# Kernel tuning notes

Hardware: AMD Instinct MI355X
Metric: run time of the kernel (lower is better)

Reference implementation:

```python
import jax, jax.numpy as jnp
import numpy as np

B, N, K, H = 2, 2048, 48, 128
NIN = 2 * H          # num_in = 2*num_hidden (ProteinMPNN wiring)
FF = 4 * H           # PositionWiseFeedForward hidden
SCALE = 30.0
EPS = 1e-5           # torch LayerNorm default eps


def _ln(x, g, b):
    m = jnp.mean(x, axis=-1, keepdims=True)
    v = jnp.mean((x - m) ** 2, axis=-1, keepdims=True)
    return (x - m) / jnp.sqrt(v + EPS) * g + b


def _gelu(x):
    return jax.nn.gelu(x, approximate=False)  # torch.nn.GELU default (erf)


def _lin(x, W, b):
    return x @ W + b


def setup_inputs() -> dict:
    key = jax.random.key(0)
    ks = jax.random.split(key, 24)
    s = 0.05
    inp = {
        "h_V": jax.random.normal(ks[0], (B, N, H), jnp.float32),
        "h_E": jax.random.normal(ks[1], (B, N, K, H), jnp.float32),
        "E_idx": jax.random.randint(ks[2], (B, N, K), 0, N, jnp.int64),
        "mask_V": jnp.ones((B, N), jnp.float32),
        "mask_attend": jnp.ones((B, N, K), jnp.float32),
        # message MLP (node update): W1 in = H + NIN = 3H
        "W1": jax.random.normal(ks[3], (3 * H, H), jnp.float32) * s,
        "b1": jnp.zeros((H,), jnp.float32),
        "W2": jax.random.normal(ks[4], (H, H), jnp.float32) * s,
        "b2": jnp.zeros((H,), jnp.float32),
        "W3": jax.random.normal(ks[5], (H, H), jnp.float32) * s,
        "b3": jnp.zeros((H,), jnp.float32),
        # PositionWiseFeedForward
        "Wd_in": jax.random.normal(ks[6], (H, FF), jnp.float32) * s,
        "bd_in": jnp.zeros((FF,), jnp.float32),
        "Wd_out": jax.random.normal(ks[7], (FF, H), jnp.float32) * s,
        "bd_out": jnp.zeros((H,), jnp.float32),
        # edge-update MLP: W11 in = H + NIN = 3H
        "W11": jax.random.normal(ks[8], (3 * H, H), jnp.float32) * s,
        "b11": jnp.zeros((H,), jnp.float32),
        "W12": jax.random.normal(ks[9], (H, H), jnp.float32) * s,
        "b12": jnp.zeros((H,), jnp.float32),
        "W13": jax.random.normal(ks[10], (H, H), jnp.float32) * s,
        "b13": jnp.zeros((H,), jnp.float32),
        # LayerNorms
        "n1g": jnp.ones((H,), jnp.float32), "n1b": jnp.zeros((H,), jnp.float32),
        "n2g": jnp.ones((H,), jnp.float32), "n2b": jnp.zeros((H,), jnp.float32),
        "n3g": jnp.ones((H,), jnp.float32), "n3b": jnp.zeros((H,), jnp.float32),
    }
    return inp


def reference(h_V, h_E, E_idx, mask_V, mask_attend,
              W1, b1, W2, b2, W3, b3,
              Wd_in, bd_in, Wd_out, bd_out,
              W11, b11, W12, b12, W13, b13,
              n1g, n1b, n2g, n2b, n3g, n3b):
    gather = jax.vmap(lambda hv, idx: hv[idx])  # [B,N,H],[B,N,K] -> [B,N,K,H]

    # --- node update: cat_neighbors_nodes + expand + 3-layer GELU MLP ---
    h_nb = gather(h_V, E_idx)                                   # [B,N,K,H]
    hV_exp = jnp.broadcast_to(h_V[:, :, None, :], h_nb.shape)   # [B,N,K,H]
    h_EV = jnp.concatenate([hV_exp, h_E, h_nb], axis=-1)        # [B,N,K,3H]
    h_msg = _lin(_gelu(_lin(_gelu(_lin(h_EV, W1, b1)), W2, b2)), W3, b3)
    h_msg = mask_attend[..., None] * h_msg
    dh = jnp.sum(h_msg, axis=-2) / SCALE                        # masked-sum reduce
    h_V = _ln(h_V + dh, n1g, n1b)

    # --- position-wise FFN ---
    dh = _lin(_gelu(_lin(h_V, Wd_in, bd_in)), Wd_out, bd_out)
    h_V = _ln(h_V + dh, n2g, n2b)
    h_V = mask_V[..., None] * h_V

    # --- edge update (not last layer) ---
    h_nb2 = gather(h_V, E_idx)
    hV_exp2 = jnp.broadcast_to(h_V[:, :, None, :], h_nb2.shape)
    h_EV2 = jnp.concatenate([hV_exp2, h_E, h_nb2], axis=-1)     # [B,N,K,3H]
    h_msg2 = _lin(_gelu(_lin(_gelu(_lin(h_EV2, W11, b11)), W12, b12)), W13, b13)
    h_E = _ln(h_E + h_msg2, n3g, n3b)
    return (h_V, h_E)
```

## Files before the change

### kernel.cpp

```cpp
#include <hip/hip_runtime.h>
#include <hip/hip_bf16.h>
#include <stdint.h>

#define XP2 264
#define MP 136
#define EPIP 132
#define FFP 520

typedef __attribute__((ext_vector_type(8))) short bf16x8;
typedef __attribute__((ext_vector_type(4))) float f32x4;

__device__ __forceinline__ f32x4 mfma16(bf16x8 a, bf16x8 b, f32x4 c) {
  return __builtin_amdgcn_mfma_f32_16x16x32_bf16(a, b, c, 0, 0, 0);
}

__device__ __forceinline__ uint16_t f2b(float f) {
  union { __hip_bfloat16 h; uint16_t u; } v;
  v.h = __float2bfloat16(f);
  return v.u;
}
__device__ __forceinline__ uint32_t pk2f(float a, float b) {
  union { __hip_bfloat162 h; uint32_t u; } v;
  v.h = __float22bfloat162_rn(make_float2(a, b));
  return v.u;
}
__device__ __forceinline__ float gelu_f(float x) {
  float u = __builtin_fmaf(x * x, 0.044715f, 1.0f);
  float e = __builtin_amdgcn_exp2f(-2.302585093f * x * u);
  return x * __builtin_amdgcn_rcpf(1.0f + e);
}

__global__ __launch_bounds__(256) void k_prep(
    const float* __restrict__ hV,
    const float* __restrict__ W1, const float* __restrict__ W2, const float* __restrict__ W3,
    const float* __restrict__ WdIn, const float* __restrict__ WdOut,
    const float* __restrict__ W11, const float* __restrict__ W12, const float* __restrict__ W13,
    uint16_t* __restrict__ hVb,
    uint16_t* __restrict__ W1t, uint16_t* __restrict__ W2t, uint16_t* __restrict__ W3t,
    uint16_t* __restrict__ WdInT, uint16_t* __restrict__ WdOutT,
    uint16_t* __restrict__ W11t, uint16_t* __restrict__ W12t, uint16_t* __restrict__ W13t) {
  int i = blockIdx.x * 256 + threadIdx.x;
  if (i < 524288) { hVb[i] = f2b(hV[i]); return; }
  int j = i - 524288;
  if (j < 49152) { int n = j / 384, k = j - n * 384; W1t[j] = f2b(W1[k * 128 + n]); return; }
  j -= 49152;
  if (j < 16384) { int n = j >> 7, k = j & 127; W2t[j] = f2b(W2[k * 128 + n]); return; }
  j -= 16384;
  if (j < 16384) { int n = j >> 7, k = j & 127; W3t[j] = f2b(W3[k * 128 + n]); return; }
  j -= 16384;
  if (j < 65536) { int n = j >> 7, k = j & 127; WdInT[j] = f2b(WdIn[k * 512 + n]); return; }
  j -= 65536;
  if (j < 65536) { int n = j >> 9, k = j & 511; WdOutT[j] = f2b(WdOut[k * 128 + n]); return; }
  j -= 65536;
  if (j < 49152) { int n = j / 384, k = j - n * 384; W11t[j] = f2b(W11[k * 128 + n]); return; }
  j -= 49152;
  if (j < 16384) { int n = j >> 7, k = j & 127; W12t[j] = f2b(W12[k * 128 + n]); return; }
  j -= 16384;
  if (j < 16384) { int n = j >> 7, k = j & 127; W13t[j] = f2b(W13[k * 128 + n]); return; }
}

__global__ __launch_bounds__(256) void k_vec(
    const uint16_t* __restrict__ Xb, const uint16_t* __restrict__ Wt,
    float* __restrict__ C) {
  const int tid = threadIdx.x;
  const int lane = tid & 63, w = tid >> 6, l15 = lane & 15, lg = lane >> 4;
  const int row0 = blockIdx.x * 64 + w * 16;
  f32x4 acc[8] = {};
#pragma unroll
  for (int ks = 0; ks < 4; ++ks) {
    bf16x8 a = *(const bf16x8*)(Xb + (row0 + l15) * 128 + ks * 32 + lg * 8);
#pragma unroll
    for (int j = 0; j < 8; ++j) {
      bf16x8 bb = *(const bf16x8*)(Wt + (j * 16 + l15) * 384 + ks * 32 + lg * 8);
      acc[j] = mfma16(a, bb, acc[j]);
    }
  }
#pragma unroll
  for (int j = 0; j < 8; ++j)
#pragma unroll
    for (int r = 0; r < 4; ++r)
      C[(row0 + lg * 4 + r) * 128 + j * 16 + l15] = acc[j][r];
}

#define BUILD_XT(GSRC)                                                              \
  do {                                                                              \
    for (int idx = tid; idx < 48 * 32; idx += 256) {                                \
      int k_ = idx >> 5;                                                            \
      int c_ = idx & 31;                                                            \
      uint4 v_;                                                                     \
      if (c_ < 16) {                                                                \
        const float* s_ = hE + (size_t)(bn * 48 + k_) * 128 + (c_ << 3);            \
        float4 f0_ = *(const float4*)s_;                                            \
        float4 f1_ = *(const float4*)(s_ + 4);                                      \
        v_ = make_uint4(pk2f(f0_.x, f0_.y), pk2f(f0_.z, f0_.w),                     \
                        pk2f(f1_.x, f1_.y), pk2f(f1_.z, f1_.w));                    \
      } else {                                                                      \
        v_ = *(const uint4*)((GSRC) + (size_t)nbr[k_] * 128 + ((c_ - 16) << 3));    \
      }                                                                             \
      *(uint4*)(xt + k_ * XP2 + (c_ << 3)) = v_;                                    \
    }                                                                               \
  } while (0)

#define LAYER256(WT, ACC)                                                           \
  do {                                                                              \
    const uint16_t* wr0_ = (WT) + (w * 32 + l15) * 384 + 128 + lg * 8;              \
    const uint16_t* wr1_ = wr0_ + 16 * 384;                                         \
    _Pragma("unroll 2") for (int ks = 0; ks < 8; ++ks) {                            \
      bf16x8 bA_ = *(const bf16x8*)(wr0_ + ks * 32);                                \
      bf16x8 bB_ = *(const bf16x8*)(wr1_ + ks * 32);                                \
      _Pragma("unroll") for (int m = 0; m < 3; ++m) {                               \
        bf16x8 a_ = *(const bf16x8*)(xt + (m * 16 + l15) * XP2 + ks * 32 + lg * 8); \
        ACC[m][0] = mfma16(a_, bA_, ACC[m][0]);                                     \
        ACC[m][1] = mfma16(a_, bB_, ACC[m][1]);                                     \
      }                                                                             \
    }                                                                               \
  } while (0)

#define LAYER128(WT, ASRC, ACC)                                                     \
  do {                                                                              \
    const uint16_t* wr0_ = (WT) + (w * 32 + l15) * 128 + lg * 8;                    \
    const uint16_t* wr1_ = wr0_ + 16 * 128;                                         \
    _Pragma("unroll") for (int ks = 0; ks < 4; ++ks) {                              \
      bf16x8 bA_ = *(const bf16x8*)(wr0_ + ks * 32);                                \
      bf16x8 bB_ = *(const bf16x8*)(wr1_ + ks * 32);                                \
      _Pragma("unroll") for (int m = 0; m < 3; ++m) {                               \
        bf16x8 a_ = *(const bf16x8*)((ASRC) + (m * 16 + l15) * MP + ks * 32 + lg * 8); \
        ACC[m][0] = mfma16(a_, bA_, ACC[m][0]);                                     \
        ACC[m][1] = mfma16(a_, bB_, ACC[m][1]);                                     \
      }                                                                              \
    }                                                                               \
  } while (0)

#define GSTORE(ACC, BIAS, DST)                                                      \
  do {                                                                              \
    float bA_ = (BIAS)[w * 32 + l15];                                               \
    float bB_ = (BIAS)[w * 32 + 16 + l15];                                          \
    _Pragma("unroll") for (int m = 0; m < 3; ++m)                                   \
    _Pragma("unroll") for (int r = 0; r < 4; ++r) {                                 \
      int row_ = m * 16 + lg * 4 + r;                                               \
      (DST)[row_ * MP + w * 32 + l15] = f2b(gelu_f(ACC[m][0][r] + bA_));            \
      (DST)[row_ * MP + w * 32 + 16 + l15] = f2b(gelu_f(ACC[m][1][r] + bB_));       \
    }                                                                               \
  } while (0)

#define ACC_INIT(ACC, CV)                                                           \
  do {                                                                              \
    float c0_ = (CV)[bn * 128 + w * 32 + l15];                                      \
    float c1_ = (CV)[bn * 128 + w * 32 + 16 + l15];                                 \
    _Pragma("unroll") for (int m = 0; m < 3; ++m) {                                 \
      ACC[m][0] = (f32x4){c0_, c0_, c0_, c0_};                                      \
      ACC[m][1] = (f32x4){c1_, c1_, c1_, c1_};                                      \
    }                                                                               \
  } while (0)

__global__ __launch_bounds__(256, 6) void k_node(
    const float* __restrict__ hV, const float* __restrict__ hE,
    const int* __restrict__ eidx, const float* __restrict__ maskA,
    const float* __restrict__ bias1, const float* __restrict__ bias2,
    const float* __restrict__ bias3,
    const float* __restrict__ g1, const float* __restrict__ be1,
    const uint16_t* __restrict__ hVb, const float* __restrict__ C1,
    const uint16_t* __restrict__ W1t, const uint16_t* __restrict__ W2t,
    const uint16_t* __restrict__ W3t,
    float* __restrict__ hV1, uint16_t* __restrict__ hV1b) {
  __shared__ __align__(16) unsigned char lds[26880];
  uint16_t* xt = (uint16_t*)lds;
  uint16_t* midA = (uint16_t*)lds;
  uint16_t* midB = (uint16_t*)(lds + 13056);
  int* nbr = (int*)(lds + 26112);
  float* dh = (float*)(lds + 26368);

  const int tid = threadIdx.x;
  const int lane = tid & 63;
  const int w = tid >> 6;
  const int l15 = lane & 15;
  const int lg = lane >> 4;
  const int bn = blockIdx.x;
  const int b = bn >> 11;

  if (tid < 48) nbr[tid] = (b << 11) + eidx[bn * 48 + tid];
  __syncthreads();

  BUILD_XT(hVb);
  __syncthreads();

  f32x4 acc1[3][2];
  ACC_INIT(acc1, C1);
  LAYER256(W1t, acc1);
  __syncthreads();
  GSTORE(acc1, bias1, midA);
  __syncthreads();

  f32x4 acc2[3][2] = {};
  LAYER128(W2t, midA, acc2);
  GSTORE(acc2, bias2, midB);
  __syncthreads();

  f32x4 acc3[3][2] = {};
  LAYER128(W3t, midB, acc3);

  {
    float bA = bias3[w * 32 + l15];
    float bB = bias3[w * 32 + 16 + l15];
    float s0 = 0.f, s1 = 0.f;
#pragma unroll
    for (int m = 0; m < 3; ++m)
#pragma unroll
      for (int r = 0; r < 4; ++r) {
        int row = m * 16 + lg * 4 + r;
        float mk = maskA[bn * 48 + row];
        s0 += (acc3[m][0][r] + bA) * mk;
        s1 += (acc3[m][1][r] + bB) * mk;
      }
    s0 += __shfl_xor(s0, 16); s0 += __shfl_xor(s0, 32);
    s1 += __shfl_xor(s1, 16); s1 += __shfl_xor(s1, 32);
    if (lg == 0) { dh[w * 32 + l15] = s0; dh[w * 32 + 16 + l15] = s1; }
  }
  __syncthreads();

  if (w == 0) {
    const float inv = 1.0f / 30.0f;
    float x0 = hV[bn * 128 + lane] + dh[lane] * inv;
    float x1 = hV[bn * 128 + 64 + lane] + dh[64 + lane] * inv;
    float s = x0 + x1, q = x0 * x0 + x1 * x1;
#pragma unroll
    for (int off = 1; off < 64; off <<= 1) {
      s += __shfl_xor(s, off);
      q += __shfl_xor(q, off);
    }
    float mean = s * (1.0f / 128.0f);
    float var = q * (1.0f / 128.0f) - mean * mean;
    float rstd = rsqrtf(var + 1e-5f);
    float y0 = (x0 - mean) * rstd * g1[lane] + be1[lane];
    float y1 = (x1 - mean) * rstd * g1[64 + lane] + be1[64 + lane];
    hV1[bn * 128 + lane] = y0;
    hV1[bn * 128 + 64 + lane] = y1;
    hV1b[bn * 128 + lane] = f2b(y0);
    hV1b[bn * 128 + 64 + lane] = f2b(y1);
  }
}

__global__ __launch_bounds__(256, 2) void k_ffn(
    const float* __restrict__ hV1, const uint16_t* __restrict__ hV1b,
    const float* __restrict__ maskV,
    const float* __restrict__ bdin, const float* __restrict__ bdout,
    const float* __restrict__ g2, const float* __restrict__ be2,
    const uint16_t* __restrict__ WdInT, const uint16_t* __restrict__ WdOutT,
    float* __restrict__ outV, uint16_t* __restrict__ hV2b) {
  __shared__ __align__(16) unsigned char lds[20992];
  uint16_t* xa = (uint16_t*)lds;
  uint16_t* mf = (uint16_t*)(lds + 4352);
  float* epi = (float*)(lds + 4352);

  const int tid = threadIdx.x;
  const int lane = tid & 63;
  const int w = tid >> 6;
  const int l15 = lane & 15;
  const int lg = lane >> 4;
  const int node0 = blockIdx.x * 16;

  {
    int row = tid >> 4, c = tid & 15;
    *(uint4*)(xa + row * 136 + (c << 3)) =
        *(const uint4*)(hV1b + (node0 + row) * 128 + (c << 3));
  }
  __syncthreads();

  f32x4 acc[8] = {};
  {
    const uint16_t* ar = xa + l15 * 136 + lg * 8;
#pragma unroll
    for (int ks = 0; ks < 4; ++ks) {
      bf16x8 a = *(const bf16x8*)(ar + ks * 32);
#pragma unroll
      for (int j = 0; j < 8; ++j) {
        bf16x8 bb = *(const bf16x8*)(WdInT + ((w * 8 + j) * 16 + l15) * 128 + ks * 32 + lg * 8);
        acc[j] = mfma16(a, bb, acc[j]);
      }
    }
  }
#pragma unroll
  for (int j = 0; j < 8; ++j) {
    int col = (w * 8 + j) * 16 + l15;
    float bs = bdin[col];
#pragma unroll
    for (int r = 0; r < 4; ++r) {
      int row = lg * 4 + r;
      mf[row * FFP + col] = f2b(gelu_f(acc[j][r] + bs));
    }
  }
  __syncthreads();

  f32x4 acc2[2] = {};
  {
    const uint16_t* mr = mf + l15 * FFP + lg * 8;
#pragma unroll 4
    for (int ks = 0; ks < 16; ++ks) {
      bf16x8 a = *(const bf16x8*)(mr + ks * 32);
#pragma unroll
      for (int t = 0; t < 2; ++t) {
        bf16x8 bb = *(const bf16x8*)(WdOutT + ((w * 2 + t) * 16 + l15) * 512 + ks * 32 + lg * 8);
        acc2[t] = mfma16(a, bb, acc2[t]);
      }
    }
  }
  __syncthreads();
#pragma unroll
  for (int t = 0; t < 2; ++t) {
    int col = (w * 2 + t) * 16 + l15;
    float bs = bdout[col];
#pragma unroll
    for (int r = 0; r < 4; ++r) {
      int row = lg * 4 + r;
      epi[row * EPIP + col] = acc2[t][r] + bs;
    }
  }
  __syncthreads();

#pragma unroll
  for (int rr = 0; rr < 4; ++rr) {
    int row = w * 4 + rr;
    int node = node0 + row;
    float x0 = epi[row * EPIP + lane] + hV1[node * 128 + lane];
    float x1 = epi[row * EPIP + 64 + lane] + hV1[node * 128 + 64 + lane];
    float s = x0 + x1, q = x0 * x0 + x1 * x1;
#pragma unroll
    for (int off = 1; off < 64; off <<= 1) {
      s += __shfl_xor(s, off);
      q += __shfl_xor(q, off);
    }
    float mean = s * (1.0f / 128.0f);
    float var = q * (1.0f / 128.0f) - mean * mean;
    float rstd = rsqrtf(var + 1e-5f);
    float mv = maskV[node];
    float y0 = mv * ((x0 - mean) * rstd * g2[lane] + be2[lane]);
    float y1 = mv * ((x1 - mean) * rstd * g2[64 + lane] + be2[64 + lane]);
    outV[node * 128 + lane] = y0;
    outV[node * 128 + 64 + lane] = y1;
    hV2b[node * 128 + lane] = f2b(y0);
    hV2b[node * 128 + 64 + lane] = f2b(y1);
  }
}

__global__ __launch_bounds__(256, 6) void k_edge(
    const float* __restrict__ hE, const int* __restrict__ eidx,
    const float* __restrict__ bias1, const float* __restrict__ bias2,
    const float* __restrict__ bias3,
    const float* __restrict__ g3, const float* __restrict__ be3,
    const uint16_t* __restrict__ hV2b, const float* __restrict__ C2,
    const uint16_t* __restrict__ W1t, const uint16_t* __restrict__ W2t,
    const uint16_t* __restrict__ W3t,
    float* __restrict__ outE) {
  __shared__ __align__(16) unsigned char lds[26304];
  uint16_t* xt = (uint16_t*)lds;
  uint16_t* midA = (uint16_t*)lds;
  uint16_t* midB = (uint16_t*)(lds + 13056);
  int* nbr = (int*)(lds + 26112);
  float* part_s = (float*)lds;
  float* part_q = (float*)(lds + 768);
  float* mstd = (float*)(lds + 1536);

  const int tid = threadIdx.x;
  const int lane = tid & 63;
  const int w = tid >> 6;
  const int l15 = lane & 15;
  const int lg = lane >> 4;
  const int bn = blockIdx.x;
  const int b = bn >> 11;

  if (tid < 48) nbr[tid] = (b << 11) + eidx[bn * 48 + tid];
  __syncthreads();

  BUILD_XT(hV2b);
  __syncthreads();

  f32x4 acc1[3][2];
  ACC_INIT(acc1, C2);
  LAYER256(W1t, acc1);
  __syncthreads();
  GSTORE(acc1, bias1, midA);
  __syncthreads();

  f32x4 acc2[3][2] = {};
  LAYER128(W2t, midA, acc2);
  GSTORE(acc2, bias2, midB);
  __syncthreads();

  f32x4 acc3[3][2] = {};
  LAYER128(W3t, midB, acc3);

  const float bA = bias3[w * 32 + l15];
  const float bB = bias3[w * 32 + 16 + l15];

  float xs0[3][4], xs1[3][4];
#pragma unroll
  for (int m = 0; m < 3; ++m)
#pragma unroll
    for (int r = 0; r < 4; ++r) {
      int row = m * 16 + lg * 4 + r;
      size_t e = (size_t)bn * 48 + row;
      xs0[m][r] = acc3[m][0][r] + bA + hE[e * 128 + w * 32 + l15];
      xs1[m][r] = acc3[m][1][r] + bB + hE[e * 128 + w * 32 + 16 + l15];
      float s = xs0[m][r] + xs1[m][r];
      float q = xs0[m][r] * xs0[m][r] + xs1[m][r] * xs1[m][r];
      s += __shfl_xor(s, 1); q += __shfl_xor(q, 1);
      s += __shfl_xor(s, 2); q += __shfl_xor(q, 2);
      s += __shfl_xor(s, 4); q += __shfl_xor(q, 4);
      s += __shfl_xor(s, 8); q += __shfl_xor(q, 8);
      if (l15 == 0) { part_s[row * 4 + w] = s; part_q[row * 4 + w] = q; }
    }
  __syncthreads();

  if (tid < 48) {
    float s = part_s[tid * 4] + part_s[tid * 4 + 1] + part_s[tid * 4 + 2] + part_s[tid * 4 + 3];
    float q = part_q[tid * 4] + part_q[tid * 4 + 1] + part_q[tid * 4 + 2] + part_q[tid * 4 + 3];
    float mean = s * (1.0f / 128.0f);
    float var = q * (1.0f / 128.0f) - mean * mean;
    mstd[tid * 2] = mean;
    mstd[tid * 2 + 1] = rsqrtf(var + 1e-5f);
  }
  __syncthreads();

  const float gA = g3[w * 32 + l15], beA = be3[w * 32 + l15];
  const float gB = g3[w * 32 + 16 + l15], beB = be3[w * 32 + 16 + l15];
#pragma unroll
  for (int m = 0; m < 3; ++m)
#pragma unroll
    for (int r = 0; r < 4; ++r) {
      int row = m * 16 + lg * 4 + r;
      size_t e = (size_t)bn * 48 + row;
      float mean = mstd[row * 2];
      float rstd = mstd[row * 2 + 1];
      outE[e * 128 + w * 32 + l15] = (xs0[m][r] - mean) * rstd * gA + beA;
      outE[e * 128 + w * 32 + 16 + l15] = (xs1[m][r] - mean) * rstd * gB + beB;
    }
}

extern "C" void kernel_launch(void* const* d_in, const int* in_sizes, int n_in,
                              void* d_out, int out_size, void* d_ws, size_t ws_size,
                              hipStream_t stream) {
  const float* hV = (const float*)d_in[0];
  const float* hE = (const float*)d_in[1];
  const int* eidx = (const int*)d_in[2];
  const float* maskV = (const float*)d_in[3];
  const float* maskA = (const float*)d_in[4];
  const float* W1 = (const float*)d_in[5];   const float* b1 = (const float*)d_in[6];
  const float* W2 = (const float*)d_in[7];   const float* b2 = (const float*)d_in[8];
  const float* W3 = (const float*)d_in[9];   const float* b3 = (const float*)d_in[10];
  const float* WdIn = (const float*)d_in[11];  const float* bdin = (const float*)d_in[12];
  const float* WdOut = (const float*)d_in[13]; const float* bdout = (const float*)d_in[14];
  const float* W11 = (const float*)d_in[15]; const float* b11 = (const float*)d_in[16];
  const float* W12 = (const float*)d_in[17]; const float* b12 = (const float*)d_in[18];
  const float* W13 = (const float*)d_in[19]; const float* b13 = (const float*)d_in[20];
  const float* n1g = (const float*)d_in[21]; const float* n1b = (const float*)d_in[22];
  const float* n2g = (const float*)d_in[23]; const float* n2b = (const float*)d_in[24];
  const float* n3g = (const float*)d_in[25]; const float* n3b = (const float*)d_in[26];

  char* ws = (char*)d_ws;
  uint16_t* hVb    = (uint16_t*)(ws + 0);
  uint16_t* W1t    = (uint16_t*)(ws + 1048576);
  uint16_t* W2t    = (uint16_t*)(ws + 1146880);
  uint16_t* W3t    = (uint16_t*)(ws + 1179648);
  uint16_t* WdInT  = (uint16_t*)(ws + 1212416);
  uint16_t* WdOutT = (uint16_t*)(ws + 1343488);
  uint16_t* W11t   = (uint16_t*)(ws + 1474560);
  uint16_t* W12t   = (uint16_t*)(ws + 1572864);
  uint16_t* W13t   = (uint16_t*)(ws + 1605632);
  float*    hV1    = (float*)(ws + 1638400);
  uint16_t* hV1b   = (uint16_t*)(ws + 3735552);
  uint16_t* hV2b   = (uint16_t*)(ws + 4784128);
  float*    C1     = (float*)(ws + 5832704);
  float*    C2     = (float*)(ws + 7929856);

  float* outV = (float*)d_out;
  float* outE = (float*)d_out + 524288;

  k_prep<<<3200, 256, 0, stream>>>(hV, W1, W2, W3, WdIn, WdOut, W11, W12, W13,
                                   hVb, W1t, W2t, W3t, WdInT, WdOutT, W11t, W12t, W13t);
  k_vec<<<64, 256, 0, stream>>>(hVb, W1t, C1);
  k_node<<<4096, 256, 0, stream>>>(hV, hE, eidx, maskA, b1, b2, b3, n1g, n1b,
                                   hVb, C1, W1t, W2t, W3t, hV1, hV1b);
  k_ffn<<<256, 256, 0, stream>>>(hV1, hV1b, maskV, bdin, bdout, n2g, n2b,
                                 WdInT, WdOutT, outV, hV2b);
  k_vec<<<64, 256, 0, stream>>>(hV2b, W11t, C2);
  k_edge<<<4096, 256, 0, stream>>>(hE, eidx, b11, b12, b13, n3g, n3b,
                                   hV2b, C2, W11t, W12t, W13t, outE);
}
```

Before: 226.1 us.

## Restructure node kernel to per-wave edge tiles with direct global operand loads

The node kernel is rewritten so each 192-thread block handles two nodes (96 edges). Each wave owns 32 edges and computes all 128 output channels in transposed form, loading hE and gathered neighbor rows directly from global memory into MFMA operands. This drops the shared LDS staging of the concatenated input and most block-wide barriers; intermediate activations go to per-wave LDS buffers. Layer-1 bias is folded into the precomputed per-node vector term in k_vec, which also affects the edge kernel. The trade-off is more accumulator registers per wave (8x2 tiles) and lower occupancy via launch bounds (192,3), plus a fragile div48 trick and hard-coded batch offset. Only a compiler fence, not a barrier, separates per-wave LDS writes and reads.

```diff
diff --git a/kernel.cpp b/kernel.cpp
--- a/kernel.cpp
+++ b/kernel.cpp
@@ -2,16 +2,21 @@
 #include <hip/hip_bf16.h>
 #include <stdint.h>
 
+#define MIDP 136
 #define XP2 264
 #define MP 136
+#define FFP 520
 #define EPIP 132
-#define FFP 520
 
 typedef __attribute__((ext_vector_type(8))) short bf16x8;
 typedef __attribute__((ext_vector_type(4))) float f32x4;
 
 __device__ __forceinline__ f32x4 mfma16(bf16x8 a, bf16x8 b, f32x4 c) {
   return __builtin_amdgcn_mfma_f32_16x16x32_bf16(a, b, c, 0, 0, 0);
+}
+
+__device__ __forceinline__ void lds_fence() {
+  asm volatile("" ::: "memory");
 }
 
 __device__ __forceinline__ uint16_t f2b(float f) {
@@ -28,6 +33,9 @@
   float u = __builtin_fmaf(x * x, 0.044715f, 1.0f);
   float e = __builtin_amdgcn_exp2f(-2.302585093f * x * u);
   return x * __builtin_amdgcn_rcpf(1.0f + e);
+}
+__device__ __forceinline__ int div48(int e) {
+  return (int)((((unsigned)e >> 4) * 0xAAABu) >> 17);
 }
 
 __global__ __launch_bounds__(256) void k_prep(
@@ -61,7 +69,7 @@
 
 __global__ __launch_bounds__(256) void k_vec(
     const uint16_t* __restrict__ Xb, const uint16_t* __restrict__ Wt,
-    float* __restrict__ C) {
+    const float* __restrict__ bias, float* __restrict__ C) {
   const int tid = threadIdx.x;
   const int lane = tid & 63, w = tid >> 6, l15 = lane & 15, lg = lane >> 4;
   const int row0 = blockIdx.x * 64 + w * 16;
@@ -76,10 +84,273 @@
     }
   }
 #pragma unroll
-  for (int j = 0; j < 8; ++j)
+  for (int j = 0; j < 8; ++j) {
+    float bs = bias[j * 16 + l15];
 #pragma unroll
     for (int r = 0; r < 4; ++r)
-      C[(row0 + lg * 4 + r) * 128 + j * 16 + l15] = acc[j][r];
+      C[(row0 + lg * 4 + r) * 128 + j * 16 + l15] = acc[j][r] + bs;
+  }
+}
+
+#define T_LAYER1(WTBL, GSRC, ACC)                                                   \
+  do {                                                                              \
+    _Pragma("unroll") for (int ks = 0; ks < 8; ++ks) {                              \
+      bf16x8 xb[2];                                                                 \
+      if (ks < 4) {                                                                 \
+        _Pragma("unroll") for (int nt = 0; nt < 2; ++nt) {                          \
+          const float* p_ = hE + (size_t)e_[nt] * 128 + ks * 32 + lg * 8;           \
+          float4 f0_ = *(const float4*)p_;                                          \
+          float4 f1_ = *(const float4*)(p_ + 4);                                    \
+          union { bf16x8 v; uint32_t u[4]; } a_;                                    \
+          a_.u[0] = pk2f(f0_.x, f0_.y); a_.u[1] = pk2f(f0_.z, f0_.w);               \
+          a_.u[2] = pk2f(f1_.x, f1_.y); a_.u[3] = pk2f(f1_.z, f1_.w);               \
+          xb[nt] = a_.v;                                                            \
+        }                                                                           \
+      } else {                                                                      \
+        _Pragma("unroll") for (int nt = 0; nt < 2; ++nt)                            \
+          xb[nt] = *(const bf16x8*)((GSRC) + (size_t)nb_[nt] * 128 +                \
+                                    (ks - 4) * 32 + lg * 8);                        \
+      }                                                                             \
+      _Pragma("unroll") for (int m = 0; m < 8; ++m) {                               \
+        bf16x8 wa_ = *(const bf16x8*)((WTBL) + (m * 16 + l15) * 384 + 128 +         \
+                                      ks * 32 + lg * 8);                            \
+        ACC[m][0] = mfma16(wa_, xb[0], ACC[m][0]);                                  \
+        ACC[m][1] = mfma16(wa_, xb[1], ACC[m][1]);                                  \
+      }                                                                             \
+    }                                                                               \
+  } while (0)
+
+#define T_GELU_TO_MID(ACC)                                                          \
+  do {                                                                              \
+    _Pragma("unroll") for (int m = 0; m < 8; ++m)                                   \
+    _Pragma("unroll") for (int nt = 0; nt < 2; ++nt) {                              \
+      uint32_t p0_ = pk2f(gelu_f(ACC[m][nt][0]), gelu_f(ACC[m][nt][1]));            \
+      uint32_t p1_ = pk2f(gelu_f(ACC[m][nt][2]), gelu_f(ACC[m][nt][3]));            \
+      uint32_t* q_ = (uint32_t*)(mid + (nt * 16 + l15) * MIDP + m * 16 + lg * 4);   \
+      q_[0] = p0_; q_[1] = p1_;                                                     \
+    }                                                                               \
+  } while (0)
+
+#define T_LAYER128(WTBL, ACC)                                                       \
+  do {                                                                              \
+    _Pragma("unroll") for (int ks = 0; ks < 4; ++ks) {                              \
+      bf16x8 xb[2];                                                                 \
+      _Pragma("unroll") for (int nt = 0; nt < 2; ++nt)                              \
+        xb[nt] = *(const bf16x8*)(mid + (nt * 16 + l15) * MIDP + ks * 32 + lg * 8); \
+      _Pragma("unroll") for (int m = 0; m < 8; ++m) {                               \
+        bf16x8 wa_ = *(const bf16x8*)((WTBL) + (m * 16 + l15) * 128 +               \
+                                      ks * 32 + lg * 8);                            \
+        ACC[m][0] = mfma16(wa_, xb[0], ACC[m][0]);                                  \
+        ACC[m][1] = mfma16(wa_, xb[1], ACC[m][1]);                                  \
+      }                                                                             \
+    }                                                                               \
+  } while (0)
+
+#define T_BIAS_INIT(ACC, BIAS)                                                      \
+  do {                                                                              \
+    _Pragma("unroll") for (int m = 0; m < 8; ++m) {                                 \
+      f32x4 v_;                                                                     \
+      _Pragma("unroll") for (int r = 0; r < 4; ++r)                                 \
+        v_[r] = (BIAS)[m * 16 + lg * 4 + r];                                        \
+      ACC[m][0] = v_; ACC[m][1] = v_;                                               \
+    }                                                                               \
+  } while (0)
+
+__global__ __launch_bounds__(192, 3) void k_node(
+    const float* __restrict__ hV, const float* __restrict__ hE,
+    const int* __restrict__ eidx, const float* __restrict__ maskA,
+    const float* __restrict__ b2, const float* __restrict__ b3,
+    const float* __restrict__ g1, const float* __restrict__ be1,
+    const uint16_t* __restrict__ hVb, const float* __restrict__ C1,
+    const uint16_t* __restrict__ W1t, const uint16_t* __restrict__ W2t,
+    const uint16_t* __restrict__ W3t,
+    float* __restrict__ hV1, uint16_t* __restrict__ hV1b) {
+  __shared__ __align__(16) unsigned char lds[29184];
+  const int tid = threadIdx.x;
+  const int lane = tid & 63;
+  const int w = tid >> 6;
+  const int l15 = lane & 15;
+  const int lg = lane >> 4;
+  uint16_t* mid = (uint16_t*)(lds + w * 8704);
+  float* dhc = (float*)(lds + 26112);
+
+  const int base = blockIdx.x * 96 + w * 32;
+  int e_[2], nb_[2];
+#pragma unroll
+  for (int nt = 0; nt < 2; ++nt) {
+    e_[nt] = base + nt * 16 + l15;
+    nb_[nt] = ((e_[nt] >= 98304) ? 2048 : 0) + eidx[e_[nt]];
+  }
+
+  f32x4 acc1[8][2];
+#pragma unroll
+  for (int nt = 0; nt < 2; ++nt) {
+    const float* cp = C1 + (size_t)div48(e_[nt]) * 128 + lg * 4;
+#pragma unroll
+    for (int m = 0; m < 8; ++m) {
+      f32x4 v;
+#pragma unroll
+      for (int r = 0; r < 4; ++r) v[r] = cp[m * 16 + r];
+      acc1[m][nt] = v;
+    }
+  }
+  T_LAYER1(W1t, hVb, acc1);
+  T_GELU_TO_MID(acc1);
+  lds_fence();
+
+  f32x4 acc2[8][2];
+  T_BIAS_INIT(acc2, b2);
+  T_LAYER128(W2t, acc2);
+  T_GELU_TO_MID(acc2);
+  lds_fence();
+
+  f32x4 acc3[8][2];
+  T_BIAS_INIT(acc3, b3);
+  T_LAYER128(W3t, acc3);
+  lds_fence();
+
+  float mk[2];
+#pragma unroll
+  for (int nt = 0; nt < 2; ++nt) mk[nt] = maskA[e_[nt]];
+#pragma unroll
+  for (int m = 0; m < 8; ++m)
+#pragma unroll
+    for (int nt = 0; nt < 2; ++nt)
+#pragma unroll
+      for (int r = 0; r < 4; ++r) {
+        float v = acc3[m][nt][r] * mk[nt];
+        v += __shfl_xor(v, 1); v += __shfl_xor(v, 2);
+        v += __shfl_xor(v, 4); v += __shfl_xor(v, 8);
+        if (l15 == 0) dhc[(w * 2 + nt) * 128 + m * 16 + lg * 4 + r] = v;
+      }
+  __syncthreads();
+
+  if (w < 2) {
+    int node = blockIdx.x * 2 + w;
+    const float* d0 = dhc + (3 * w) * 128;
+    float dhA = d0[lane] + d0[128 + lane] + d0[256 + lane];
+    float dhB = d0[64 + lane] + d0[192 + lane] + d0[320 + lane];
+    const float inv = 1.0f / 30.0f;
+    float x0 = hV[node * 128 + lane] + dhA * inv;
+    float x1 = hV[node * 128 + 64 + lane] + dhB * inv;
+    float s = x0 + x1, q = x0 * x0 + x1 * x1;
+#pragma unroll
+    for (int off = 1; off < 64; off <<= 1) {
+      s += __shfl_xor(s, off);
+      q += __shfl_xor(q, off);
+    }
+    float mean = s * (1.0f / 128.0f);
+    float var = q * (1.0f / 128.0f) - mean * mean;
+    float rstd = rsqrtf(var + 1e-5f);
+    float y0 = (x0 - mean) * rstd * g1[lane] + be1[lane];
+    float y1 = (x1 - mean) * rstd * g1[64 + lane] + be1[64 + lane];
+    hV1[node * 128 + lane] = y0;
+    hV1[node * 128 + 64 + lane] = y1;
+    hV1b[node * 128 + lane] = f2b(y0);
+    hV1b[node * 128 + 64 + lane] = f2b(y1);
+  }
+}
+
+__global__ __launch_bounds__(256, 2) void k_ffn(
+    const float* __restrict__ hV1, const uint16_t* __restrict__ hV1b,
+    const float* __restrict__ maskV,
+    const float* __restrict__ bdin, const float* __restrict__ bdout,
+    const float* __restrict__ g2, const float* __restrict__ be2,
+    const uint16_t* __restrict__ WdInT, const uint16_t* __restrict__ WdOutT,
+    float* __restrict__ outV, uint16_t* __restrict__ hV2b) {
+  __shared__ __align__(16) unsigned char lds[20992];
+  uint16_t* xa = (uint16_t*)lds;
+  uint16_t* mf = (uint16_t*)(lds + 4352);
+  float* epi = (float*)(lds + 4352);
+
+  const int tid = threadIdx.x;
+  const int lane = tid & 63;
+  const int w = tid >> 6;
+  const int l15 = lane & 15;
+  const int lg = lane >> 4;
+  const int node0 = blockIdx.x * 16;
+
+  {
+    int row = tid >> 4, c = tid & 15;
+    *(uint4*)(xa + row * 136 + (c << 3)) =
+        *(const uint4*)(hV1b + (node0 + row) * 128 + (c << 3));
+  }
+  __syncthreads();
+
+  f32x4 acc[8] = {};
+  {
+    const uint16_t* ar = xa + l15 * 136 + lg * 8;
+#pragma unroll
+    for (int ks = 0; ks < 4; ++ks) {
+      bf16x8 a = *(const bf16x8*)(ar + ks * 32);
+#pragma unroll
+      for (int j = 0; j < 8; ++j) {
+        bf16x8 bb = *(const bf16x8*)(WdInT + ((w * 8 + j) * 16 + l15) * 128 + ks * 32 + lg * 8);
+        acc[j] = mfma16(a, bb, acc[j]);
+      }
+    }
+  }
+#pragma unroll
+  for (int j = 0; j < 8; ++j) {
+    int col = (w * 8 + j) * 16 + l15;
+    float bs = bdin[col];
+#pragma unroll
+    for (int r = 0; r < 4; ++r) {
+      int row = lg * 4 + r;
+      mf[row * FFP + col] = f2b(gelu_f(acc[j][r] + bs));
+    }
+  }
+  __syncthreads();
+
+  f32x4 acc2[2] = {};
+  {
+    const uint16_t* mr = mf + l15 * FFP + lg * 8;
+#pragma unroll 4
+    for (int ks = 0; ks < 16; ++ks) {
+      bf16x8 a = *(const bf16x8*)(mr + ks * 32);
+#pragma unroll
+      for (int t = 0; t < 2; ++t) {
+        bf16x8 bb = *(const bf16x8*)(WdOutT + ((w * 2 + t) * 16 + l15) * 512 + ks * 32 + lg * 8);
+        acc2[t] = mfma16(a, bb, acc2[t]);
+      }
+    }
+  }
+  __syncthreads();
+#pragma unroll
+  for (int t = 0; t < 2; ++t) {
+    int col = (w * 2 + t) * 16 + l15;
+    float bs = bdout[col];
+#pragma unroll
+    for (int r = 0; r < 4; ++r) {
+      int row = lg * 4 + r;
+      epi[row * EPIP + col] = acc2[t][r] + bs;
+    }
+  }
+  __syncthreads();
+
+#pragma unroll
+  for (int rr = 0; rr < 4; ++rr) {
+    int row = w * 4 + rr;
+    int node = node0 + row;
+    float x0 = epi[row * EPIP + lane] + hV1[node * 128 + lane];
+    float x1 = epi[row * EPIP + 64 + lane] + hV1[node * 128 + 64 + lane];
+    float s = x0 + x1, q = x0 * x0 + x1 * x1;
+#pragma unroll
+    for (int off = 1; off < 64; off <<= 1) {
+      s += __shfl_xor(s, off);
+      q += __shfl_xor(q, off);
+    }
+    float mean = s * (1.0f / 128.0f);
+    float var = q * (1.0f / 128.0f) - mean * mean;
+    float rstd = rsqrtf(var + 1e-5f);
+    float mv = maskV[node];
+    float y0 = mv * ((x0 - mean) * rstd * g2[lane] + be2[lane]);
+    float y1 = mv * ((x1 - mean) * rstd * g2[64 + lane] + be2[64 + lane]);
+    outV[node * 128 + lane] = y0;
+    outV[node * 128 + 64 + lane] = y1;
+    hV2b[node * 128 + lane] = f2b(y0);
+    hV2b[node * 128 + 64 + lane] = f2b(y1);
+  }
 }
 
 #define BUILD_XT(GSRC)                                                              \
@@ -143,6 +414,16 @@
     }                                                                               \
   } while (0)
 
+#define GSTORE0(ACC, DST)                                                           \
+  do {                                                                              \
+    _Pragma("unroll") for (int m = 0; m < 3; ++m)                                   \
+    _Pragma("unroll") for (int r = 0; r < 4; ++r) {                                 \
+      int row_ = m * 16 + lg * 4 + r;                                               \
+      (DST)[row_ * MP + w * 32 + l15] = f2b(gelu_f(ACC[m][0][r]));                  \
+      (DST)[row_ * MP + w * 32 + 16 + l15] = f2b(gelu_f(ACC[m][1][r]));             \
+    }                                                                               \
+  } while (0)
+
 #define ACC_INIT(ACC, CV)                                                           \
   do {                                                                              \
     float c0_ = (CV)[bn * 128 + w * 32 + l15];                                      \
@@ -153,199 +434,9 @@
     }                                                                               \
   } while (0)
 
-__global__ __launch_bounds__(256, 6) void k_node(
-    const float* __restrict__ hV, const float* __restrict__ hE,
-    const int* __restrict__ eidx, const float* __restrict__ maskA,
-    const float* __restrict__ bias1, const float* __restrict__ bias2,
-    const float* __restrict__ bias3,
-    const float* __restrict__ g1, const float* __restrict__ be1,
-    const uint16_t* __restrict__ hVb, const float* __restrict__ C1,
-    const uint16_t* __restrict__ W1t, const uint16_t* __restrict__ W2t,
-    const uint16_t* __restrict__ W3t,
-    float* __restrict__ hV1, uint16_t* __restrict__ hV1b) {
-  __shared__ __align__(16) unsigned char lds[26880];
-  uint16_t* xt = (uint16_t*)lds;
-  uint16_t* midA = (uint16_t*)lds;
-  uint16_t* midB = (uint16_t*)(lds + 13056);
-  int* nbr = (int*)(lds + 26112);
-  float* dh = (float*)(lds + 26368);
-
-  const int tid = threadIdx.x;
-  const int lane = tid & 63;
-  const int w = tid >> 6;
-  const int l15 = lane & 15;
-  const int lg = lane >> 4;
-  const int bn = blockIdx.x;
-  const int b = bn >> 11;
-
-  if (tid < 48) nbr[tid] = (b << 11) + eidx[bn * 48 + tid];
-  __syncthreads();
-
-  BUILD_XT(hVb);
-  __syncthreads();
-
-  f32x4 acc1[3][2];
-  ACC_INIT(acc1, C1);
-  LAYER256(W1t, acc1);
-  __syncthreads();
-  GSTORE(acc1, bias1, midA);
-  __syncthreads();
-
-  f32x4 acc2[3][2] = {};
-  LAYER128(W2t, midA, acc2);
-  GSTORE(acc2, bias2, midB);
-  __syncthreads();
-
-  f32x4 acc3[3][2] = {};
-  LAYER128(W3t, midB, acc3);
-
-  {
-    float bA = bias3[w * 32 + l15];
-    float bB = bias3[w * 32 + 16 + l15];
-    float s0 = 0.f, s1 = 0.f;
-#pragma unroll
-    for (int m = 0; m < 3; ++m)
-#pragma unroll
-      for (int r = 0; r < 4; ++r) {
-        int row = m * 16 + lg * 4 + r;
-        float mk = maskA[bn * 48 + row];
-        s0 += (acc3[m][0][r] + bA) * mk;
-        s1 += (acc3[m][1][r] + bB) * mk;
-      }
-    s0 += __shfl_xor(s0, 16); s0 += __shfl_xor(s0, 32);
-    s1 += __shfl_xor(s1, 16); s1 += __shfl_xor(s1, 32);
-    if (lg == 0) { dh[w * 32 + l15] = s0; dh[w * 32 + 16 + l15] = s1; }
-  }
-  __syncthreads();
-
-  if (w == 0) {
-    const float inv = 1.0f / 30.0f;
-    float x0 = hV[bn * 128 + lane] + dh[lane] * inv;
-    float x1 = hV[bn * 128 + 64 + lane] + dh[64 + lane] * inv;
-    float s = x0 + x1, q = x0 * x0 + x1 * x1;
-#pragma unroll
-    for (int off = 1; off < 64; off <<= 1) {
-      s += __shfl_xor(s, off);
-      q += __shfl_xor(q, off);
-    }
-    float mean = s * (1.0f / 128.0f);
-    float var = q * (1.0f / 128.0f) - mean * mean;
-    float rstd = rsqrtf(var + 1e-5f);
-    float y0 = (x0 - mean) * rstd * g1[lane] + be1[lane];
-    float y1 = (x1 - mean) * rstd * g1[64 + lane] + be1[64 + lane];
-    hV1[bn * 128 + lane] = y0;
-    hV1[bn * 128 + 64 + lane] = y1;
-    hV1b[bn * 128 + lane] = f2b(y0);
-    hV1b[bn * 128 + 64 + lane] = f2b(y1);
-  }
-}
-
-__global__ __launch_bounds__(256, 2) void k_ffn(
-    const float* __restrict__ hV1, const uint16_t* __restrict__ hV1b,
-    const float* __restrict__ maskV,
-    const float* __restrict__ bdin, const float* __restrict__ bdout,
-    const float* __restrict__ g2, const float* __restrict__ be2,
-    const uint16_t* __restrict__ WdInT, const uint16_t* __restrict__ WdOutT,
-    float* __restrict__ outV, uint16_t* __restrict__ hV2b) {
-  __shared__ __align__(16) unsigned char lds[20992];
-  uint16_t* xa = (uint16_t*)lds;
-  uint16_t* mf = (uint16_t*)(lds + 4352);
-  float* epi = (float*)(lds + 4352);
-
-  const int tid = threadIdx.x;
-  const int lane = tid & 63;
-  const int w = tid >> 6;
-  const int l15 = lane & 15;
-  const int lg = lane >> 4;
-  const int node0 = blockIdx.x * 16;
-
-  {
-    int row = tid >> 4, c = tid & 15;
-    *(uint4*)(xa + row * 136 + (c << 3)) =
-        *(const uint4*)(hV1b + (node0 + row) * 128 + (c << 3));
-  }
-  __syncthreads();
-
-  f32x4 acc[8] = {};
-  {
-    const uint16_t* ar = xa + l15 * 136 + lg * 8;
-#pragma unroll
-    for (int ks = 0; ks < 4; ++ks) {
-      bf16x8 a = *(const bf16x8*)(ar + ks * 32);
-#pragma unroll
-      for (int j = 0; j < 8; ++j) {
-        bf16x8 bb = *(const bf16x8*)(WdInT + ((w * 8 + j) * 16 + l15) * 128 + ks * 32 + lg * 8);
-        acc[j] = mfma16(a, bb, acc[j]);
-      }
-    }
-  }
-#pragma unroll
-  for (int j = 0; j < 8; ++j) {
-    int col = (w * 8 + j) * 16 + l15;
-    float bs = bdin[col];
-#pragma unroll
-    for (int r = 0; r < 4; ++r) {
-      int row = lg * 4 + r;
-      mf[row * FFP + col] = f2b(gelu_f(acc[j][r] + bs));
-    }
-  }
-  __syncthreads();
-
-  f32x4 acc2[2] = {};
-  {
-    const uint16_t* mr = mf + l15 * FFP + lg * 8;
-#pragma unroll 4
-    for (int ks = 0; ks < 16; ++ks) {
-      bf16x8 a = *(const bf16x8*)(mr + ks * 32);
-#pragma unroll
-      for (int t = 0; t < 2; ++t) {
-        bf16x8 bb = *(const bf16x8*)(WdOutT + ((w * 2 + t) * 16 + l15) * 512 + ks * 32 + lg * 8);
-        acc2[t] = mfma16(a, bb, acc2[t]);
-      }
-    }
-  }
-  __syncthreads();
-#pragma unroll
-  for (int t = 0; t < 2; ++t) {
-    int col = (w * 2 + t) * 16 + l15;
-    float bs = bdout[col];
-#pragma unroll
-    for (int r = 0; r < 4; ++r) {
-      int row = lg * 4 + r;
-      epi[row * EPIP + col] = acc2[t][r] + bs;
-    }
-  }
-  __syncthreads();
-
-#pragma unroll
-  for (int rr = 0; rr < 4; ++rr) {
-    int row = w * 4 + rr;
-    int node = node0 + row;
-    float x0 = epi[row * EPIP + lane] + hV1[node * 128 + lane];
-    float x1 = epi[row * EPIP + 64 + lane] + hV1[node * 128 + 64 + lane];
-    float s = x0 + x1, q = x0 * x0 + x1 * x1;
-#pragma unroll
-    for (int off = 1; off < 64; off <<= 1) {
-      s += __shfl_xor(s, off);
-      q += __shfl_xor(q, off);
-    }
-    float mean = s * (1.0f / 128.0f);
-    float var = q * (1.0f / 128.0f) - mean * mean;
-    float rstd = rsqrtf(var + 1e-5f);
-    float mv = maskV[node];
-    float y0 = mv * ((x0 - mean) * rstd * g2[lane] + be2[lane]);
-    float y1 = mv * ((x1 - mean) * rstd * g2[64 + lane] + be2[64 + lane]);
-    outV[node * 128 + lane] = y0;
-    outV[node * 128 + 64 + lane] = y1;
-    hV2b[node * 128 + lane] = f2b(y0);
-    hV2b[node * 128 + 64 + lane] = f2b(y1);
-  }
-}
-
 __global__ __launch_bounds__(256, 6) void k_edge(
     const float* __restrict__ hE, const int* __restrict__ eidx,
-    const float* __restrict__ bias1, const float* __restrict__ bias2,
-    const float* __restrict__ bias3,
+    const float* __restrict__ bias2, const float* __restrict__ bias3,
     const float* __restrict__ g3, const float* __restrict__ be3,
     const uint16_t* __restrict__ hV2b, const float* __restrict__ C2,
     const uint16_t* __restrict__ W1t, const uint16_t* __restrict__ W2t,
@@ -378,7 +469,7 @@
   ACC_INIT(acc1, C2);
   LAYER256(W1t, acc1);
   __syncthreads();
-  GSTORE(acc1, bias1, midA);
+  GSTORE0(acc1, midA);
   __syncthreads();
 
   f32x4 acc2[3][2] = {};
@@ -477,12 +568,12 @@
 
   k_prep<<<3200, 256, 0, stream>>>(hV, W1, W2, W3, WdIn, WdOut, W11, W12, W13,
                                    hVb, W1t, W2t, W3t, WdInT, WdOutT, W11t, W12t, W13t);
-  k_vec<<<64, 256, 0, stream>>>(hVb, W1t, C1);
-  k_node<<<4096, 256, 0, stream>>>(hV, hE, eidx, maskA, b1, b2, b3, n1g, n1b,
+  k_vec<<<64, 256, 0, stream>>>(hVb, W1t, b1, C1);
+  k_node<<<2048, 192, 0, stream>>>(hV, hE, eidx, maskA, b2, b3, n1g, n1b,
                                    hVb, C1, W1t, W2t, W3t, hV1, hV1b);
   k_ffn<<<256, 256, 0, stream>>>(hV1, hV1b, maskV, bdin, bdout, n2g, n2b,
                                  WdInT, WdOutT, outV, hV2b);
-  k_vec<<<64, 256, 0, stream>>>(hV2b, W11t, C2);
-  k_edge<<<4096, 256, 0, stream>>>(hE, eidx, b11, b12, b13, n3g, n3b,
+  k_vec<<<64, 256, 0, stream>>>(hV2b, W11t, b11, C2);
+  k_edge<<<4096, 256, 0, stream>>>(hE, eidx, b12, b13, n3g, n3b,
                                    hV2b, C2, W11t, W12t, W13t, outE);
 }
```

New measurement: 298.2 us. 1.32x slower.
